# Optimization experiments

Measured on AMD Instinct MI355X. Metric: run time of the kernel, lower is better.

## Reference

```python
import jax, jax.numpy as jnp
import numpy as np

B, N, DIN, DOUT, DA = 8, 2048, 128, 128, 2
NEG_SLOPE = 0.2


def setup_inputs() -> dict:
    key = jax.random.key(0)
    k = jax.random.split(key, 7)
    x = jax.random.normal(k[0], (B, N, DIN), dtype=jnp.float32)
    mask = jax.random.randint(k[1], (B, N, N), 0, 2, dtype=jnp.int32)
    s = 1.0 / np.sqrt(DIN)
    Wr = jax.random.uniform(k[2], (DA, DIN), jnp.float32, -s, s)      # linear_row.weight
    Wc = jax.random.uniform(k[3], (DA, DIN), jnp.float32, -s, s)      # linear_col.weight
    sa = 1.0 / np.sqrt(2 * DA)
    Wcat = jax.random.uniform(k[4], (2 * DA,), jnp.float32, -sa, sa)  # linear_concat.weight [1, 2*DA] flattened
    Wx = jax.random.uniform(k[5], (DOUT, DIN), jnp.float32, -s, s)    # linear_x.weight
    bx = jax.random.uniform(k[6], (DOUT,), jnp.float32, -s, s)        # linear_x.bias
    return {"x": x, "mask": mask, "Wr": Wr, "Wc": Wc, "Wcat": Wcat, "Wx": Wx, "bx": bx}


def reference(x, mask, Wr, Wc, Wcat, Wx, bx):
    # Row/col projections to tiny attention dim: [B, N, DA]
    row = jnp.einsum('bnd,ad->bna', x, Wr)
    col = jnp.einsum('bnd,ad->bna', x, Wc)
    # Concat scoring: e_ij = linear_concat(LeakyReLU(cat(row_i, col_j)))
    # decomposes as a1 . LR(row_i) + a2 . LR(col_j) -- avoids materializing [B,N,N,2*DA]
    a1, a2 = Wcat[:DA], Wcat[DA:]
    lr_row = jax.nn.leaky_relu(row, NEG_SLOPE) @ a1   # [B, N]
    lr_col = jax.nn.leaky_relu(col, NEG_SLOPE) @ a2   # [B, N]
    e = lr_row[:, :, None] + lr_col[:, None, :]       # [B, N, N]
    # Masked softmax over columns j
    e = jnp.where(mask > 0, e, jnp.float32(-1e9))
    atten = jax.nn.softmax(e, axis=-1)                # [B, N, N]
    # Value projection + combine
    xv = jnp.einsum('bnd,od->bno', x, Wx) + bx        # [B, N, DOUT]
    out = jnp.einsum('bij,bjo->bio', atten, xv)       # [B, N, DOUT]
    return out
```

## Files before the change

### kernel.cpp

```cpp
#include <hip/hip_runtime.h>


typedef __bf16 bf16x8 __attribute__((ext_vector_type(8)));
typedef __bf16 bf16x4 __attribute__((ext_vector_type(4)));
typedef float  f32x4  __attribute__((ext_vector_type(4)));
typedef int    i32x4  __attribute__((ext_vector_type(4)));

#define MFMA_BF16(a, b, c) __builtin_amdgcn_mfma_f32_16x16x32_bf16((a), (b), (c), 0, 0, 0)

static __device__ __forceinline__ bf16x8 cvt8(f32x4 a, f32x4 b) {
  bf16x8 r;
  r[0] = (__bf16)a[0]; r[1] = (__bf16)a[1]; r[2] = (__bf16)a[2]; r[3] = (__bf16)a[3];
  r[4] = (__bf16)b[0]; r[5] = (__bf16)b[1]; r[6] = (__bf16)b[2]; r[7] = (__bf16)b[3];
  return r;
}

__global__ __launch_bounds__(256) void prep_kernel(
    const float* __restrict__ x, const float* __restrict__ Wc,
    const float* __restrict__ Wcat, const float* __restrict__ Wx,
    const float* __restrict__ bx, __bf16* __restrict__ u,
    __bf16* __restrict__ wcol)
{
  __shared__ __bf16 lds[8192];
  const int blk = blockIdx.x;
  const int b = blk >> 5, mt = blk & 31;
  const int wv = threadIdx.x >> 6, lane = threadIdx.x & 63;
  const int np = lane & 15, G = lane >> 4;
  const int r0 = mt * 64 + wv * 16;

  const float* xp = x + ((size_t)(b * 2048 + r0 + np)) * 128 + G * 8;
  bf16x8 af[4];
#pragma unroll
  for (int kk = 0; kk < 4; ++kk) {
    f32x4 x0 = *(const f32x4*)(xp + kk * 32);
    f32x4 x1 = *(const f32x4*)(xp + kk * 32 + 4);
    af[kk] = cvt8(x0, x1);
  }

  f32x4 acc[8], accC;
#pragma unroll
  for (int n = 0; n < 8; ++n) { acc[n][0] = 0.f; acc[n][1] = 0.f; acc[n][2] = 0.f; acc[n][3] = 0.f; }
  accC[0] = accC[1] = accC[2] = accC[3] = 0.f;

#pragma unroll
  for (int n = 0; n < 8; ++n) {
    const float* wp = Wx + (n * 16 + np) * 128 + G * 8;
#pragma unroll
    for (int kk = 0; kk < 4; ++kk) {
      f32x4 w0 = *(const f32x4*)(wp + kk * 32);
      f32x4 w1 = *(const f32x4*)(wp + kk * 32 + 4);
      acc[n] = MFMA_BF16(af[kk], cvt8(w0, w1), acc[n]);
    }
  }
#pragma unroll
  for (int kk = 0; kk < 4; ++kk) {
    bf16x8 bf;
    if (np < 2) {
      const float* cp = Wc + np * 128 + kk * 32 + G * 8;
      f32x4 c0 = *(const f32x4*)cp;
      f32x4 c1 = *(const f32x4*)(cp + 4);
      bf = cvt8(c0, c1);
    } else {
#pragma unroll
      for (int j = 0; j < 8; ++j) bf[j] = (__bf16)0.0f;
    }
    accC = MFMA_BF16(af[kk], bf, accC);
  }

  const float a20 = Wcat[2], a21 = Wcat[3];
  float wexp[4];
#pragma unroll
  for (int r = 0; r < 4; ++r) {
    float c0 = __shfl(accC[r], lane & 48);
    float c1 = __shfl(accC[r], (lane & 48) | 1);
    c0 = c0 > 0.f ? c0 : 0.2f * c0;
    c1 = c1 > 0.f ? c1 : 0.2f * c1;
    wexp[r] = __expf(c0 * a20 + c1 * a21);
  }
  if (np == 0) {
    bf16x4 w4;
#pragma unroll
    for (int r = 0; r < 4; ++r) w4[r] = (__bf16)wexp[r];
    *(bf16x4*)(wcol + (size_t)b * 2048 + r0 + 4 * G) = w4;
  }

  const int t_rel = wv >> 1;
  const int g_store = (wv & 1) * 2 + (G >> 1);
  const int j0 = (G & 1) * 4;
#pragma unroll
  for (int n = 0; n < 8; ++n) {
    float bxv = bx[n * 16 + np];
    bf16x4 v;
#pragma unroll
    for (int r = 0; r < 4; ++r) v[r] = (__bf16)(wexp[r] * (acc[n][r] + bxv));
    *(bf16x4*)(&lds[(t_rel * 8 + n) * 512 + g_store * 128 + np * 8 + j0]) = v;
  }
  __syncthreads();
  __bf16* dst = u + ((size_t)(b * 64 + mt * 2)) * 4096;
#pragma unroll
  for (int it = 0; it < 4; ++it) {
    int s = it * 256 + threadIdx.x;
    ((i32x4*)dst)[s] = ((const i32x4*)lds)[s];
  }
}

__global__ __launch_bounds__(256) void attn_kernel(
    const int* __restrict__ mask, const __bf16* __restrict__ u,
    const __bf16* __restrict__ wcol, float* __restrict__ out)
{
  const int b = blockIdx.x & 7, mt = blockIdx.x >> 3;
  const int wv = threadIdx.x >> 6, lane = threadIdx.x & 63;
  const int np = lane & 15, G = lane >> 4;
  const int row0 = mt * 64 + wv * 16;
  const long long N = 2048;

  const int* mp = mask + ((size_t)b * N + row0 + np) * N + G * 8;
  const __bf16* up = u + (size_t)b * 64 * 4096 + lane * 8;
  const __bf16* wp = wcol + (size_t)b * 2048 + G * 8;

  f32x4 acc[9];
#pragma unroll
  for (int n = 0; n < 9; ++n) { acc[n][0] = 0.f; acc[n][1] = 0.f; acc[n][2] = 0.f; acc[n][3] = 0.f; }

  i32x4 m0A, m1A, m0B, m1B;
  bf16x8 ufA[8], ufB[8], wfA, wfB;

#define LOADS(t, m0, m1, uf, wf)                                         \
  do {                                                                   \
    const int* mpt = mp + (t) * 32;                                      \
    m0 = *(const i32x4*)mpt;                                             \
    m1 = *(const i32x4*)(mpt + 4);                                       \
    const __bf16* upt = up + (t) * 4096;                                 \
    _Pragma("unroll")                                                    \
    for (int n = 0; n < 8; ++n) uf[n] = *(const bf16x8*)(upt + n * 512); \
    wf = *(const bf16x8*)(wp + (t) * 32);                                \
  } while (0)

#define COMPS(m0, m1, uf, wf)                                            \
  do {                                                                   \
    const __bf16 ONE = (__bf16)1.0f, ZER = (__bf16)0.0f;                 \
    bf16x8 af;                                                           \
    af[0] = m0[0] ? ONE : ZER; af[1] = m0[1] ? ONE : ZER;                \
    af[2] = m0[2] ? ONE : ZER; af[3] = m0[3] ? ONE : ZER;                \
    af[4] = m1[0] ? ONE : ZER; af[5] = m1[1] ? ONE : ZER;                \
    af[6] = m1[2] ? ONE : ZER; af[7] = m1[3] ? ONE : ZER;                \
    bf16x8 wfrag;                                                        \
    _Pragma("unroll")                                                    \
    for (int j = 0; j < 8; ++j) wfrag[j] = (np == 0) ? wf[j] : ZER;      \
    _Pragma("unroll")                                                    \
    for (int n = 0; n < 8; ++n) acc[n] = MFMA_BF16(af, uf[n], acc[n]);   \
    acc[8] = MFMA_BF16(af, wfrag, acc[8]);                               \
  } while (0)

  LOADS(0, m0A, m1A, ufA, wfA);
  LOADS(1, m0B, m1B, ufB, wfB);
  for (int t = 0; t < 64; t += 2) {
    COMPS(m0A, m1A, ufA, wfA);
    if (t + 2 < 64) LOADS(t + 2, m0A, m1A, ufA, wfA);
    COMPS(m0B, m1B, ufB, wfB);
    if (t + 3 < 64) LOADS(t + 3, m0B, m1B, ufB, wfB);
  }
#undef LOADS
#undef COMPS

#pragma unroll
  for (int r = 0; r < 4; ++r) {
    float den = __shfl(acc[8][r], lane & 48);
    float inv = 1.0f / den;
    float* op = out + ((size_t)b * N + row0 + 4 * G + r) * 128 + np;
#pragma unroll
    for (int n = 0; n < 8; ++n) op[n * 16] = acc[n][r] * inv;
  }
}

extern "C" void kernel_launch(void* const* d_in, const int* in_sizes, int n_in,
                              void* d_out, int out_size, void* d_ws, size_t ws_size,
                              hipStream_t stream) {
  const float* x    = (const float*)d_in[0];
  const int*   mask = (const int*)d_in[1];
  const float* Wc   = (const float*)d_in[3];
  const float* Wcat = (const float*)d_in[4];
  const float* Wx   = (const float*)d_in[5];
  const float* bx   = (const float*)d_in[6];
  float* out = (float*)d_out;

  const size_t U_BYTES = (size_t)8 * 64 * 4096 * 2;
  if (ws_size < U_BYTES + 8 * 2048 * 2) return;
  __bf16* u    = (__bf16*)d_ws;
  __bf16* wcol = (__bf16*)((char*)d_ws + U_BYTES);

  prep_kernel<<<256, 256, 0, stream>>>(x, Wc, Wcat, Wx, bx, u, wcol);
  attn_kernel<<<256, 256, 0, stream>>>(mask, u, wcol, out);
}
```

Measured before the change: 237.9 us.

## Restructure attention kernel with LDS multi-buffered async loads and 32-row tiles

The attention kernel now stages mask and value tiles into LDS through global_load_lds with a 4-deep ring buffer, explicit vmcnt waits and barriers, and an XOR swizzle on mask rows. Each block covers 32 rows, with waves splitting the output columns, and the grid doubles to 512 blocks. The softmax denominator is accumulated with scalar FMAs and shuffle reductions instead of an extra MFMA. The intent is to hide HBM latency on the mask stream and raise occupancy, at the cost of barrier overhead and each block re-reading the value tiles.

```diff
diff --git a/kernel.cpp b/kernel.cpp
--- a/kernel.cpp
+++ b/kernel.cpp
@@ -5,8 +5,14 @@
 typedef __bf16 bf16x4 __attribute__((ext_vector_type(4)));
 typedef float  f32x4  __attribute__((ext_vector_type(4)));
 typedef int    i32x4  __attribute__((ext_vector_type(4)));
+typedef unsigned int u32;
 
 #define MFMA_BF16(a, b, c) __builtin_amdgcn_mfma_f32_16x16x32_bf16((a), (b), (c), 0, 0, 0)
+
+#define GLOAD_LDS16(gp, lp)                                                     \
+  __builtin_amdgcn_global_load_lds(                                             \
+      (const __attribute__((address_space(1))) void*)(gp),                      \
+      (__attribute__((address_space(3))) void*)(lp), 16, 0, 0)
 
 static __device__ __forceinline__ bf16x8 cvt8(f32x4 a, f32x4 b) {
   bf16x8 r;
@@ -108,68 +114,99 @@
     const int* __restrict__ mask, const __bf16* __restrict__ u,
     const __bf16* __restrict__ wcol, float* __restrict__ out)
 {
-  const int b = blockIdx.x & 7, mt = blockIdx.x >> 3;
+  __shared__ char smem[4 * 12288 + 4096];
+  char* wbuf = smem + 49152;
+  const int b = blockIdx.x & 7, rt = blockIdx.x >> 3;
   const int wv = threadIdx.x >> 6, lane = threadIdx.x & 63;
   const int np = lane & 15, G = lane >> 4;
-  const int row0 = mt * 64 + wv * 16;
-  const long long N = 2048;
-
-  const int* mp = mask + ((size_t)b * N + row0 + np) * N + G * 8;
-  const __bf16* up = u + (size_t)b * 64 * 4096 + lane * 8;
-  const __bf16* wp = wcol + (size_t)b * 2048 + G * 8;
-
-  f32x4 acc[9];
-#pragma unroll
-  for (int n = 0; n < 9; ++n) { acc[n][0] = 0.f; acc[n][1] = 0.f; acc[n][2] = 0.f; acc[n][3] = 0.f; }
-
-  i32x4 m0A, m1A, m0B, m1B;
-  bf16x8 ufA[8], ufB[8], wfA, wfB;
-
-#define LOADS(t, m0, m1, uf, wf)                                         \
-  do {                                                                   \
-    const int* mpt = mp + (t) * 32;                                      \
-    m0 = *(const i32x4*)mpt;                                             \
-    m1 = *(const i32x4*)(mpt + 4);                                       \
-    const __bf16* upt = up + (t) * 4096;                                 \
-    _Pragma("unroll")                                                    \
-    for (int n = 0; n < 8; ++n) uf[n] = *(const bf16x8*)(upt + n * 512); \
-    wf = *(const bf16x8*)(wp + (t) * 32);                                \
+  const int row0 = rt * 32;
+  const int n0 = wv * 2, n1 = n0 + 1;
+  const int swzB = (np & 7) << 4;
+
+  const char* gmask = (const char*)(mask + ((size_t)b * 2048 + row0) * 2048);
+  const char* gu    = (const char*)u + (size_t)b * 64 * 8192;
+  const char* gw    = (const char*)(wcol + (size_t)b * 2048);
+
+  const int srow = lane >> 3;
+  const long long moff = (size_t)(8 * wv + srow) * 8192 + (((lane & 7) ^ srow) << 4);
+
+  f32x4 acc[2][2];
+#pragma unroll
+  for (int mi = 0; mi < 2; ++mi)
+#pragma unroll
+    for (int n = 0; n < 2; ++n) { acc[mi][n][0] = 0.f; acc[mi][n][1] = 0.f; acc[mi][n][2] = 0.f; acc[mi][n][3] = 0.f; }
+  float den[2] = {0.f, 0.f};
+
+#define STAGE(it, nb)                                                          \
+  do {                                                                         \
+    char* mb_ = smem + (nb) * 12288;                                           \
+    GLOAD_LDS16(gmask + moff + (it) * 128, mb_ + wv * 1024);                   \
+    const char* up_ = gu + (size_t)(it) * 8192 + lane * 16;                    \
+    GLOAD_LDS16(up_ + (2 * wv) * 1024, mb_ + 4096 + (2 * wv) * 1024);          \
+    GLOAD_LDS16(up_ + (2 * wv + 1) * 1024, mb_ + 4096 + (2 * wv + 1) * 1024);  \
   } while (0)
 
-#define COMPS(m0, m1, uf, wf)                                            \
-  do {                                                                   \
-    const __bf16 ONE = (__bf16)1.0f, ZER = (__bf16)0.0f;                 \
-    bf16x8 af;                                                           \
-    af[0] = m0[0] ? ONE : ZER; af[1] = m0[1] ? ONE : ZER;                \
-    af[2] = m0[2] ? ONE : ZER; af[3] = m0[3] ? ONE : ZER;                \
-    af[4] = m1[0] ? ONE : ZER; af[5] = m1[1] ? ONE : ZER;                \
-    af[6] = m1[2] ? ONE : ZER; af[7] = m1[3] ? ONE : ZER;                \
-    bf16x8 wfrag;                                                        \
-    _Pragma("unroll")                                                    \
-    for (int j = 0; j < 8; ++j) wfrag[j] = (np == 0) ? wf[j] : ZER;      \
-    _Pragma("unroll")                                                    \
-    for (int n = 0; n < 8; ++n) acc[n] = MFMA_BF16(af, uf[n], acc[n]);   \
-    acc[8] = MFMA_BF16(af, wfrag, acc[8]);                               \
+#define CONSUME(it, nb)                                                        \
+  do {                                                                         \
+    const char* mb = smem + (nb) * 12288;                                      \
+    const char* ub = mb + 4096;                                                \
+    bf16x8 W = *(const bf16x8*)(wbuf + (it) * 64 + G * 16);                    \
+    float wf[8];                                                               \
+    _Pragma("unroll")                                                          \
+    for (int j = 0; j < 8; ++j) wf[j] = (float)W[j];                           \
+    bf16x8 U0 = *(const bf16x8*)(ub + n0 * 1024 + lane * 16);                  \
+    bf16x8 U1 = *(const bf16x8*)(ub + n1 * 1024 + lane * 16);                  \
+    _Pragma("unroll")                                                          \
+    for (int mi = 0; mi < 2; ++mi) {                                           \
+      const char* rp = mb + (mi * 16 + np) * 128;                              \
+      i32x4 ma = *(const i32x4*)(rp + ((G * 32) ^ swzB));                      \
+      i32x4 mz = *(const i32x4*)(rp + ((G * 32 + 16) ^ swzB));                 \
+      union { u32 w[4]; bf16x8 v; } A;                                         \
+      A.w[0] = (ma[0] ? 0x3F80u : 0u) | (ma[1] ? 0x3F800000u : 0u);            \
+      A.w[1] = (ma[2] ? 0x3F80u : 0u) | (ma[3] ? 0x3F800000u : 0u);            \
+      A.w[2] = (mz[0] ? 0x3F80u : 0u) | (mz[1] ? 0x3F800000u : 0u);            \
+      A.w[3] = (mz[2] ? 0x3F80u : 0u) | (mz[3] ? 0x3F800000u : 0u);            \
+      float d = den[mi];                                                       \
+      d += ma[0] ? wf[0] : 0.f; d += ma[1] ? wf[1] : 0.f;                      \
+      d += ma[2] ? wf[2] : 0.f; d += ma[3] ? wf[3] : 0.f;                      \
+      d += mz[0] ? wf[4] : 0.f; d += mz[1] ? wf[5] : 0.f;                      \
+      d += mz[2] ? wf[6] : 0.f; d += mz[3] ? wf[7] : 0.f;                      \
+      den[mi] = d;                                                             \
+      acc[mi][0] = MFMA_BF16(A.v, U0, acc[mi][0]);                             \
+      acc[mi][1] = MFMA_BF16(A.v, U1, acc[mi][1]);                             \
+    }                                                                          \
   } while (0)
 
-  LOADS(0, m0A, m1A, ufA, wfA);
-  LOADS(1, m0B, m1B, ufB, wfB);
-  for (int t = 0; t < 64; t += 2) {
-    COMPS(m0A, m1A, ufA, wfA);
-    if (t + 2 < 64) LOADS(t + 2, m0A, m1A, ufA, wfA);
-    COMPS(m0B, m1B, ufB, wfB);
-    if (t + 3 < 64) LOADS(t + 3, m0B, m1B, ufB, wfB);
-  }
-#undef LOADS
-#undef COMPS
-
-#pragma unroll
-  for (int r = 0; r < 4; ++r) {
-    float den = __shfl(acc[8][r], lane & 48);
-    float inv = 1.0f / den;
-    float* op = out + ((size_t)b * N + row0 + 4 * G + r) * 128 + np;
-#pragma unroll
-    for (int n = 0; n < 8; ++n) op[n * 16] = acc[n][r] * inv;
+  GLOAD_LDS16(gw + wv * 1024 + lane * 16, wbuf + wv * 1024);
+  STAGE(0, 0); STAGE(1, 1); STAGE(2, 2);
+
+  for (int it = 0; it <= 61; ++it) {
+    asm volatile("s_waitcnt vmcnt(6)" ::: "memory");
+    __builtin_amdgcn_s_barrier();
+    CONSUME(it, it & 3);
+    if (it <= 60) STAGE(it + 3, (it + 3) & 3);
+  }
+  asm volatile("s_waitcnt vmcnt(3)" ::: "memory");
+  __builtin_amdgcn_s_barrier();
+  CONSUME(62, 2);
+  asm volatile("s_waitcnt vmcnt(0)" ::: "memory");
+  __builtin_amdgcn_s_barrier();
+  CONSUME(63, 3);
+#undef STAGE
+#undef CONSUME
+
+#pragma unroll
+  for (int mi = 0; mi < 2; ++mi) {
+    float dr = den[mi] + __shfl_xor(den[mi], 16);
+    dr += __shfl_xor(dr, 32);
+#pragma unroll
+    for (int r = 0; r < 4; ++r) {
+      float dv = __shfl(dr, 4 * G + r);
+      float inv = 1.0f / dv;
+      float* op = out + ((size_t)b * 2048 + row0 + mi * 16 + 4 * G + r) * 128 + np;
+      op[n0 * 16] = acc[mi][0][r] * inv;
+      op[n1 * 16] = acc[mi][1][r] * inv;
+    }
   }
 }
 
@@ -190,5 +227,5 @@
   __bf16* wcol = (__bf16*)((char*)d_ws + U_BYTES);
 
   prep_kernel<<<256, 256, 0, stream>>>(x, Wc, Wcat, Wx, bx, u, wcol);
-  attn_kernel<<<256, 256, 0, stream>>>(mask, u, wcol, out);
-}
+  attn_kernel<<<512, 256, 0, stream>>>(mask, u, wcol, out);
+}
```

New measurement: 232.1 us. 2.4% less time.
